# Performance work log

Hardware: AMD Instinct MI355X
Metric: run time of the kernel (lower is better)

Reference implementation:

```python
import jax, jax.numpy as jnp
import numpy as np

N = 16384      # total atoms (8 proteins x ~2048)
E = 524288     # N * max_neighbors(32)
B = 8          # graphs
F_IN = 26      # 20 residue types + 6 atom types
D = 128        # node_dim
H = 256        # hidden_dim
OUT = 64       # output_dim
L = 4          # n_layers
N_RBF = 16
CUTOFF = 10.0


def setup_inputs() -> dict:
    key = jax.random.key(0)
    ks = jax.random.split(key, 24)
    s = 0.05
    inp = {
        "positions": jax.random.normal(ks[0], (N, 3), jnp.float32) * 10.0,
        "node_features": jax.random.normal(ks[1], (N, F_IN), jnp.float32),
        "edge_index": jax.random.randint(ks[2], (2, E), 0, N, jnp.int32),
        "batch": jnp.sort(jax.random.randint(ks[3], (N,), 0, B, jnp.int32)),
        # node embedding MLP
        "emb_W1": jax.random.normal(ks[4], (F_IN, D), jnp.float32) * s,
        "emb_b1": jnp.zeros((D,), jnp.float32),
        "emb_W2": jax.random.normal(ks[5], (D, D), jnp.float32) * s,
        "emb_b2": jnp.zeros((D,), jnp.float32),
        # per-layer message MLP: [2D + n_rbf] -> H -> D
        "msg_W1": jax.random.normal(ks[6], (L, 2 * D + N_RBF, H), jnp.float32) * s,
        "msg_b1": jnp.zeros((L, H), jnp.float32),
        "msg_W2": jax.random.normal(ks[7], (L, H, D), jnp.float32) * s,
        "msg_b2": jnp.zeros((L, D), jnp.float32),
        # per-layer update MLP: [2D] -> H -> D (residual)
        "upd_W1": jax.random.normal(ks[8], (L, 2 * D, H), jnp.float32) * s,
        "upd_b1": jnp.zeros((L, H), jnp.float32),
        "upd_W2": jax.random.normal(ks[9], (L, H, D), jnp.float32) * s,
        "upd_b2": jnp.zeros((L, D), jnp.float32),
        # readout MLP: D -> H -> OUT
        "r_W1": jax.random.normal(ks[10], (D, H), jnp.float32) * s,
        "r_b1": jnp.zeros((H,), jnp.float32),
        "r_W2": jax.random.normal(ks[11], (H, OUT), jnp.float32) * s,
        "r_b2": jnp.zeros((OUT,), jnp.float32),
    }
    return inp


def _mlp2(x, W1, b1, W2, b2):
    return jax.nn.silu(x @ W1 + b1) @ W2 + b2


def _edge_rbf(positions, src, dst):
    rel = positions[dst] - positions[src]                      # (E,3)
    d = jnp.sqrt(jnp.sum(rel * rel, axis=-1) + 1e-12)          # (E,)
    centers = jnp.linspace(0.0, CUTOFF, N_RBF, dtype=positions.dtype)
    width = CUTOFF / N_RBF
    rbf = jnp.exp(-((d[:, None] - centers) ** 2) / (2.0 * width * width))  # (E,n_rbf)
    env = 0.5 * (jnp.cos(jnp.pi * d / CUTOFF) + 1.0) * (d < CUTOFF)        # cosine cutoff
    return rbf * env[:, None]


def reference(positions, node_features, edge_index, batch,
              emb_W1, emb_b1, emb_W2, emb_b2,
              msg_W1, msg_b1, msg_W2, msg_b2,
              upd_W1, upd_b1, upd_W2, upd_b2,
              r_W1, r_b1, r_W2, r_b2):
    src, dst = edge_index[0], edge_index[1]
    h = _mlp2(node_features, emb_W1, emb_b1, emb_W2, emb_b2)   # (N,D)
    ef = _edge_rbf(positions, src, dst)                        # (E,n_rbf)
    for i in range(L):
        m_in = jnp.concatenate([h[src], h[dst], ef], axis=-1)  # (E,2D+n_rbf)
        m = _mlp2(m_in, msg_W1[i], msg_b1[i], msg_W2[i], msg_b2[i])  # (E,D)
        agg = jax.ops.segment_sum(m, dst, num_segments=N)      # (N,D)
        u_in = jnp.concatenate([h, agg], axis=-1)              # (N,2D)
        h = h + _mlp2(u_in, upd_W1[i], upd_b1[i], upd_W2[i], upd_b2[i])
    # mean readout per graph
    counts = jax.ops.segment_sum(jnp.ones((N,), h.dtype), batch, num_segments=B)
    g = jax.ops.segment_sum(h, batch, num_segments=B) / jnp.maximum(counts, 1.0)[:, None]
    return _mlp2(g, r_W1, r_b1, r_W2, r_b2)                    # (B,OUT)
```

## Files before the change

kernel.cpp:

```cpp
#include <hip/hip_runtime.h>
#include <math.h>

#define NATOMS 16384
#define NEDGES 524288
#define NLAYERS 4
#define TE 64

typedef __bf16 bf16x8 __attribute__((ext_vector_type(8)));
typedef __bf16 bf16x4 __attribute__((ext_vector_type(4)));
typedef __bf16 bf16x2 __attribute__((ext_vector_type(2)));
typedef float f32x4 __attribute__((ext_vector_type(4)));

__device__ __forceinline__ float silu_f(float x) {
  return x * __builtin_amdgcn_rcpf(1.0f + __expf(-x));
}

__global__ __launch_bounds__(1024) void scan_kernel(
    const int* __restrict__ counts, int* __restrict__ cursor,
    float* __restrict__ degf)
{
  __shared__ int s_tot[1024];
  int tid = threadIdx.x;
  int v[16];
  {
    const int4* cp = (const int4*)(counts + tid * 16);
    int4 a = cp[0], b = cp[1], c = cp[2], d = cp[3];
    v[0]=a.x; v[1]=a.y; v[2]=a.z; v[3]=a.w;
    v[4]=b.x; v[5]=b.y; v[6]=b.z; v[7]=b.w;
    v[8]=c.x; v[9]=c.y; v[10]=c.z; v[11]=c.w;
    v[12]=d.x; v[13]=d.y; v[14]=d.z; v[15]=d.w;
  }
  int tot = 0;
  #pragma unroll
  for (int i = 0; i < 16; i++) tot += v[i];
  s_tot[tid] = tot;
  __syncthreads();
  for (int off = 1; off < 1024; off <<= 1) {
    int t = (tid >= off) ? s_tot[tid - off] : 0;
    __syncthreads();
    s_tot[tid] += t;
    __syncthreads();
  }
  int run = s_tot[tid] - tot;
  #pragma unroll
  for (int i = 0; i < 16; i++) {
    cursor[tid * 16 + i] = run;
    degf[tid * 16 + i] = (float)v[i];
    run += v[i];
  }
}

__global__ __launch_bounds__(256) void scatter_rbf_kernel(
    const int* __restrict__ src, const int* __restrict__ dst,
    int* __restrict__ cursor, const float* __restrict__ pos,
    int* __restrict__ esrc, int* __restrict__ edst,
    __bf16* __restrict__ efb)
{
  int e = blockIdx.x * 256 + threadIdx.x;
  int s = src[e], d = dst[e];
  int p = atomicAdd(&cursor[d], 1);
  esrc[p] = s;
  edst[p] = d;
  float dx = pos[d * 3 + 0] - pos[s * 3 + 0];
  float dy = pos[d * 3 + 1] - pos[s * 3 + 1];
  float dz = pos[d * 3 + 2] - pos[s * 3 + 2];
  float dist = sqrtf(dx * dx + dy * dy + dz * dz + 1e-12f);
  float env = (dist < 10.0f)
                  ? 0.5f * (cosf(3.14159265358979f * dist * 0.1f) + 1.0f)
                  : 0.0f;
  bf16x8 o0, o1;
  #pragma unroll
  for (int i = 0; i < 16; i++) {
    float c = (10.0f / 15.0f) * (float)i;
    float t = dist - c;
    float v = env * __expf(-t * t * 1.28f);
    if (i < 8) o0[i] = (__bf16)v; else o1[i - 8] = (__bf16)v;
  }
  *(bf16x8*)(efb + (size_t)p * 16 + 0) = o0;
  *(bf16x8*)(efb + (size_t)p * 16 + 8) = o1;
}

#define NB_PREP (801 * NLAYERS)
#define NB_HIST (NEDGES / 256)
#define NB_EMB  (NATOMS / 2)

__global__ __launch_bounds__(256) void front_kernel(
    const float* __restrict__ mW1, const float* __restrict__ mW2,
    const float* __restrict__ uW1, const float* __restrict__ uW2,
    const float* __restrict__ mb2,
    __bf16* __restrict__ W1at, __bf16* __restrict__ W1bt,
    __bf16* __restrict__ B2c, __bf16* __restrict__ uW1ft,
    __bf16* __restrict__ uW2t, float* __restrict__ b2u,
    const int* __restrict__ dstI, int* __restrict__ counts,
    const float* __restrict__ x, const float* __restrict__ eW1,
    const float* __restrict__ eb1, const float* __restrict__ eW2,
    const float* __restrict__ eb2, float* __restrict__ h,
    __bf16* __restrict__ hb)
{
  __shared__ float xs[2][26];
  __shared__ float hid[2][132];
  int bxf = blockIdx.x, tid = threadIdx.x;

  if (bxf < NB_PREP) {
    long l = bxf / 801;
    int bx = bxf - (int)l * 801;
    if (bx < 128) {
      int i = bx * 256 + tid;
      int n = i >> 7, k = i & 127;
      W1at[l * (256L * 128) + i] = (__bf16)mW1[l * (272L * 256) + (size_t)k * 256 + n];
    } else if (bx < 256) {
      int i = (bx - 128) * 256 + tid;
      int n = i >> 7, k = i & 127;
      W1bt[l * (256L * 128) + i] = (__bf16)mW1[l * (272L * 256) + (size_t)(128 + k) * 256 + n];
    } else if (bx < 288) {
      int i = (bx - 256) * 256 + tid;
      int c = i >> 5, k = i & 31;
      float v = (k < 16) ? mW1[l * (272L * 256) + (size_t)(256 + k) * 256 + c] : 0.0f;
      B2c[l * (256L * 32) + i] = (__bf16)v;
    } else if (bx < 672) {
      int k = bx - 288;
      int n = tid;
      float v;
      if (k < 128) {
        v = uW1[l * 65536 + (size_t)k * 256 + n];
      } else {
        int r = k - 128;
        v = 0.0f;
        for (int j = 0; j < 128; j++)
          v += mW2[(l * 256 + r) * 128 + j] * uW1[l * 65536 + (size_t)(128 + j) * 256 + n];
      }
      uW1ft[l * (256L * 384) + (size_t)n * 384 + k] = (__bf16)v;
    } else if (bx < 800) {
      int i = (bx - 672) * 256 + tid;
      int n = i >> 8, k = i & 255;
      uW2t[l * (128L * 256) + i] = (__bf16)uW2[l * (256L * 128) + (size_t)k * 128 + n];
    } else {
      int c = tid;
      float acc = 0.0f;
      for (int j = 0; j < 128; j++)
        acc += mb2[l * 128 + j] * uW1[l * 65536 + (size_t)(128 + j) * 256 + c];
      b2u[l * 256 + c] = acc;
    }
  } else if (bxf < NB_PREP + NB_HIST) {
    int e = (bxf - NB_PREP) * 256 + tid;
    atomicAdd(&counts[dstI[e]], 1);
  } else {
    int nb = bxf - (NB_PREP + NB_HIST);
    int hf = tid >> 7, j = tid & 127;
    int n = nb * 2 + hf;
    if (j < 26) xs[hf][j] = x[(size_t)n * 26 + j];
    __syncthreads();
    float acc = eb1[j];
    #pragma unroll
    for (int k = 0; k < 26; k++) acc += xs[hf][k] * eW1[k * 128 + j];
    hid[hf][j] = silu_f(acc);
    __syncthreads();
    float acc2 = eb2[j];
    #pragma unroll 8
    for (int k = 0; k < 128; k++) acc2 += hid[hf][k] * eW2[k * 128 + j];
    h[(size_t)n * 128 + j] = acc2;
    hb[(size_t)n * 128 + j] = (__bf16)acc2;
  }
}

__global__ __launch_bounds__(256) void zprep_kernel(
    const __bf16* __restrict__ hb, const float* __restrict__ b1,
    const __bf16* __restrict__ W1at, const __bf16* __restrict__ W1bt,
    __bf16* __restrict__ z1b, __bf16* __restrict__ z2b, float* __restrict__ aggH)
{
  __shared__ __bf16 s_n[64][136];
  int tid = threadIdx.x, n0 = blockIdx.x * 64;
  {
    int n = tid >> 2, t4 = tid & 3;
    const bf16x8* hr = (const bf16x8*)(hb + (size_t)(n0 + n) * 128);
    #pragma unroll
    for (int i = 0; i < 4; i++)
      *(bf16x8*)&s_n[n][t4 * 8 + 32 * i] = hr[t4 + 4 * i];
  }
  {
    float4 zz = make_float4(0.f, 0.f, 0.f, 0.f);
    float4* ap = (float4*)(aggH + (size_t)n0 * 256);
    for (int i = tid; i < 64 * 256 / 4; i += 256) ap[i] = zz;
  }
  __syncthreads();
  const int wv = tid >> 6, ln = tid & 63, lc = ln & 15, qd = ln >> 4;
  for (int cp = 0; cp < 2; cp++) {
    f32x4 aA[4][2], aB[4][2];
    #pragma unroll
    for (int nt = 0; nt < 2; nt++) {
      float bv = b1[cp * 128 + wv * 32 + nt * 16 + lc];
      #pragma unroll
      for (int mt = 0; mt < 4; mt++) {
        aA[mt][nt][0] = 0.f; aA[mt][nt][1] = 0.f;
        aA[mt][nt][2] = 0.f; aA[mt][nt][3] = 0.f;
        aB[mt][nt][0] = bv; aB[mt][nt][1] = bv;
        aB[mt][nt][2] = bv; aB[mt][nt][3] = bv;
      }
    }
    #pragma unroll
    for (int kt = 0; kt < 4; kt++) {
      bf16x8 af[4];
      #pragma unroll
      for (int mt = 0; mt < 4; mt++)
        af[mt] = *(const bf16x8*)&s_n[mt * 16 + lc][kt * 32 + qd * 8];
      bf16x8 bwA[2], bwB[2];
      #pragma unroll
      for (int nt = 0; nt < 2; nt++) {
        int c = cp * 128 + wv * 32 + nt * 16 + lc;
        bwA[nt] = *(const bf16x8*)(W1at + (size_t)c * 128 + kt * 32 + qd * 8);
        bwB[nt] = *(const bf16x8*)(W1bt + (size_t)c * 128 + kt * 32 + qd * 8);
      }
      #pragma unroll
      for (int mt = 0; mt < 4; mt++)
        #pragma unroll
        for (int nt = 0; nt < 2; nt++) {
          aA[mt][nt] = __builtin_amdgcn_mfma_f32_16x16x32_bf16(af[mt], bwA[nt], aA[mt][nt], 0, 0, 0);
          aB[mt][nt] = __builtin_amdgcn_mfma_f32_16x16x32_bf16(af[mt], bwB[nt], aB[mt][nt], 0, 0, 0);
        }
    }
    #pragma unroll
    for (int mt = 0; mt < 4; mt++)
      #pragma unroll
      for (int nt = 0; nt < 2; nt++) {
        int c = cp * 128 + wv * 32 + nt * 16 + lc;
        #pragma unroll
        for (int r = 0; r < 4; r++) {
          int n = n0 + mt * 16 + qd * 4 + r;
          z1b[(size_t)n * 256 + c] = (__bf16)aA[mt][nt][r];
          z2b[(size_t)n * 256 + c] = (__bf16)aB[mt][nt][r];
        }
      }
  }
}

#define MS_EF_OFF   33792
#define MS_SRC_OFF  36864
#define MS_DST_OFF  37120
#define MS_MASK_OFF 37376
#define MS_BYTES    37392

__global__ __launch_bounds__(256, 4) void msg_mfma_kernel(
    const __bf16* __restrict__ z1b, const __bf16* __restrict__ z2b,
    const __bf16* __restrict__ efb,
    const int* __restrict__ esrc, const int* __restrict__ edst,
    const __bf16* __restrict__ B2c, float* __restrict__ aggH)
{
  __shared__ __align__(16) char smem[MS_BYTES];
  __bf16 (*s_hT)[66] = (__bf16(*)[66])(smem);
  __bf16 (*s_ef)[24] = (__bf16(*)[24])(smem + MS_EF_OFF);
  int* s_src = (int*)(smem + MS_SRC_OFF);
  int* s_dst = (int*)(smem + MS_DST_OFF);
  unsigned int* s_mask = (unsigned int*)(smem + MS_MASK_OFF);

  int tid = threadIdx.x, e0 = blockIdx.x * TE;

  if (tid < TE) {
    int d = edst[e0 + tid];
    s_dst[tid] = d;
    int dp = (tid == 0) ? (d ^ 1) : edst[e0 + tid - 1];
    unsigned long long mb = __ballot(d != dp);
    if (tid == 0) { s_mask[0] = (unsigned int)mb; s_mask[1] = (unsigned int)(mb >> 32); }
  } else if (tid < 2 * TE) {
    s_src[tid - TE] = esrc[e0 + tid - TE];
  }
  {
    int e = tid >> 2, t4 = tid & 3;
    if (t4 < 2)
      *(bf16x8*)&s_ef[e][t4 * 8] =
          *(const bf16x8*)(efb + (size_t)(e0 + e) * 16 + t4 * 8);
  }
  __syncthreads();

  const int wv = tid >> 6, ln = tid & 63, lc = ln & 15, qd = ln >> 4;

  bf16x8 bI;
  #pragma unroll
  for (int j = 0; j < 8; j++)
    bI[j] = (__bf16)((lc == (qd & 1) * 8 + j) ? 1.0f : 0.0f);

  const __bf16* pz[4];
  #pragma unroll
  for (int mt = 0; mt < 4; mt++) {
    int m = mt * 16 + lc;
    int row = (qd < 2) ? s_src[m] : s_dst[m];
    pz[mt] = ((qd < 2) ? z1b : z2b) + (size_t)row * 256 + (qd & 1) * 8;
  }

  #pragma unroll
  for (int hf = 0; hf < 2; hf++) {
    const int cb = hf * 128 + wv * 32;
    bf16x8 bw[2];
    #pragma unroll
    for (int nt = 0; nt < 2; nt++)
      bw[nt] = *(const bf16x8*)(B2c + (size_t)(cb + nt * 16 + lc) * 32 + qd * 8);

    #pragma unroll
    for (int mt = 0; mt < 4; mt++) {
      bf16x8 aef = *(const bf16x8*)&s_ef[mt * 16 + lc][(qd & 1) * 8];
      #pragma unroll
      for (int nt = 0; nt < 2; nt++) {
        bf16x8 az = *(const bf16x8*)(pz[mt] + cb + nt * 16);
        f32x4 z; z[0] = 0.f; z[1] = 0.f; z[2] = 0.f; z[3] = 0.f;
        f32x4 acc = __builtin_amdgcn_mfma_f32_16x16x32_bf16(az, bI, z, 0, 0, 0);
        acc = __builtin_amdgcn_mfma_f32_16x16x32_bf16(aef, bw[nt], acc, 0, 0, 0);
        bf16x2 p0, p1;
        p0[0] = (__bf16)silu_f(acc[0]); p0[1] = (__bf16)silu_f(acc[1]);
        p1[0] = (__bf16)silu_f(acc[2]); p1[1] = (__bf16)silu_f(acc[3]);
        __bf16* wp = &s_hT[cb + nt * 16 + lc][mt * 16 + qd * 4];
        *(bf16x2*)wp = p0;
        *(bf16x2*)(wp + 2) = p1;
      }
    }
  }
  __syncthreads();

  {
    const unsigned int mlo = __builtin_amdgcn_readfirstlane(s_mask[0]);
    const unsigned int mhi = __builtin_amdgcn_readfirstlane(s_mask[1]);
    int j = tid;
    float acc = 0.0f;
    int cur = s_dst[0];
    #pragma unroll 8
    for (int i = 0; i < 64; i += 2) {
      bf16x2 p = *(const bf16x2*)&s_hT[j][i];
      bool b0 = (i < 32) ? ((mlo >> i) & 1u) : ((mhi >> (i - 32)) & 1u);
      int i1 = i + 1;
      bool b1 = (i1 < 32) ? ((mlo >> i1) & 1u) : ((mhi >> (i1 - 32)) & 1u);
      if (i > 0 && b0) {
        atomicAdd(&aggH[(size_t)cur * 256 + j], acc);
        acc = 0.0f; cur = s_dst[i];
      }
      acc += (float)p[0];
      if (b1) {
        atomicAdd(&aggH[(size_t)cur * 256 + j], acc);
        acc = 0.0f; cur = s_dst[i1];
      }
      acc += (float)p[1];
    }
    atomicAdd(&aggH[(size_t)cur * 256 + j], acc);
  }
}

__global__ __launch_bounds__(512, 2) void upd_mfma_kernel(
    float* __restrict__ h, __bf16* __restrict__ hb,
    float* __restrict__ aggH, const float* __restrict__ degf,
    const __bf16* __restrict__ uW1ft, const float* __restrict__ b1,
    const float* __restrict__ b2u,
    const __bf16* __restrict__ uW2t, const float* __restrict__ b2,
    int do_z, const float* __restrict__ nb1,
    const __bf16* __restrict__ nW1at, const __bf16* __restrict__ nW1bt,
    __bf16* __restrict__ z1b, __bf16* __restrict__ z2b)
{
  __shared__ __bf16 s_u[64][392];
  __shared__ __bf16 s_uh[64][264];
  int tid = threadIdx.x, n0 = blockIdx.x * 64;
  {
    int n = tid >> 3, t8 = tid & 7;
    const bf16x8* hr = (const bf16x8*)(hb + (size_t)(n0 + n) * 128);
    #pragma unroll
    for (int i = 0; i < 2; i++)
      *(bf16x8*)&s_u[n][t8 * 8 + 64 * i] = hr[t8 + 8 * i];
    const float* sr = aggH + (size_t)(n0 + n) * 256;
    #pragma unroll
    for (int i = 0; i < 4; i++) {
      int col = t8 * 8 + i * 64;
      float4 a = *(const float4*)(sr + col);
      float4 b = *(const float4*)(sr + col + 4);
      bf16x8 o;
      o[0] = (__bf16)a.x; o[1] = (__bf16)a.y; o[2] = (__bf16)a.z; o[3] = (__bf16)a.w;
      o[4] = (__bf16)b.x; o[5] = (__bf16)b.y; o[6] = (__bf16)b.z; o[7] = (__bf16)b.w;
      *(bf16x8*)&s_u[n][128 + col] = o;
    }
  }
  __syncthreads();
  const int wv = tid >> 6, ln = tid & 63, lc = ln & 15, qd = ln >> 4;

  float dg[4][4];
  #pragma unroll
  for (int mt = 0; mt < 4; mt++)
    #pragma unroll
    for (int r = 0; r < 4; r++)
      dg[mt][r] = degf[n0 + mt * 16 + qd * 4 + r];

  {
    f32x4 acc1[4][2];
    #pragma unroll
    for (int nt = 0; nt < 2; nt++) {
      int c = wv * 32 + nt * 16 + lc;
      float bv = b1[c];
      float b2uv = b2u[c];
      #pragma unroll
      for (int mt = 0; mt < 4; mt++)
        #pragma unroll
        for (int r = 0; r < 4; r++)
          acc1[mt][nt][r] = bv + dg[mt][r] * b2uv;
    }
    #pragma unroll
    for (int kt = 0; kt < 12; kt++) {
      bf16x8 af[4];
      #pragma unroll
      for (int mt = 0; mt < 4; mt++)
        af[mt] = *(const bf16x8*)&s_u[mt * 16 + lc][kt * 32 + qd * 8];
      bf16x8 bw[2];
      #pragma unroll
      for (int nt = 0; nt < 2; nt++)
        bw[nt] = *(const bf16x8*)(uW1ft +
                 (size_t)(wv * 32 + nt * 16 + lc) * 384 + kt * 32 + qd * 8);
      #pragma unroll
      for (int mt = 0; mt < 4; mt++)
        #pragma unroll
        for (int nt = 0; nt < 2; nt++)
          acc1[mt][nt] = __builtin_amdgcn_mfma_f32_16x16x32_bf16(af[mt], bw[nt], acc1[mt][nt], 0, 0, 0);
    }
    #pragma unroll
    for (int mt = 0; mt < 4; mt++)
      #pragma unroll
      for (int nt = 0; nt < 2; nt++) {
        int cc = wv * 32 + nt * 16 + lc;
        #pragma unroll
        for (int r = 0; r < 4; r++)
          s_uh[mt * 16 + qd * 4 + r][cc] = (__bf16)silu_f(acc1[mt][nt][r]);
      }
  }
  __syncthreads();

  const int ow = wv * 16 + lc;
  f32x4 acc2[4];
  {
    float bv = b2[ow];
    #pragma unroll
    for (int mt = 0; mt < 4; mt++) {
      acc2[mt][0] = bv; acc2[mt][1] = bv; acc2[mt][2] = bv; acc2[mt][3] = bv;
    }
  }
  #pragma unroll
  for (int kt = 0; kt < 8; kt++) {
    bf16x8 a2[4];
    #pragma unroll
    for (int mt = 0; mt < 4; mt++)
      a2[mt] = *(const bf16x8*)&s_uh[mt * 16 + lc][kt * 32 + qd * 8];
    bf16x8 b2w = *(const bf16x8*)(uW2t + (size_t)ow * 256 + kt * 32 + qd * 8);
    #pragma unroll
    for (int mt = 0; mt < 4; mt++)
      acc2[mt] = __builtin_amdgcn_mfma_f32_16x16x32_bf16(a2[mt], b2w, acc2[mt], 0, 0, 0);
  }

  #pragma unroll
  for (int mt = 0; mt < 4; mt++)
    #pragma unroll
    for (int r = 0; r < 4; r++) {
      int n = n0 + mt * 16 + qd * 4 + r;
      float v = h[(size_t)n * 128 + ow] + acc2[mt][r];
      h[(size_t)n * 128 + ow] = v;
      hb[(size_t)n * 128 + ow] = (__bf16)v;
    }

  if (do_z) {
    __syncthreads();
    {
      float4 zz = make_float4(0.f, 0.f, 0.f, 0.f);
      float4* ap = (float4*)(aggH + (size_t)n0 * 256);
      for (int i = tid; i < 64 * 256 / 4; i += 512) ap[i] = zz;
      int n = tid >> 3, t8 = tid & 7;
      const bf16x8* hr = (const bf16x8*)(hb + (size_t)(n0 + n) * 128);
      #pragma unroll
      for (int i = 0; i < 2; i++)
        *(bf16x8*)&s_u[n][t8 * 8 + 64 * i] = hr[t8 + 8 * i];
    }
    __syncthreads();
    f32x4 aA[4][2], aB[4][2];
    #pragma unroll
    for (int nt = 0; nt < 2; nt++) {
      float bv = nb1[wv * 32 + nt * 16 + lc];
      #pragma unroll
      for (int mt = 0; mt < 4; mt++) {
        aA[mt][nt][0] = 0.f; aA[mt][nt][1] = 0.f;
        aA[mt][nt][2] = 0.f; aA[mt][nt][3] = 0.f;
        aB[mt][nt][0] = bv; aB[mt][nt][1] = bv;
        aB[mt][nt][2] = bv; aB[mt][nt][3] = bv;
      }
    }
    #pragma unroll
    for (int kt = 0; kt < 4; kt++) {
      bf16x8 af[4];
      #pragma unroll
      for (int mt = 0; mt < 4; mt++)
        af[mt] = *(const bf16x8*)&s_u[mt * 16 + lc][kt * 32 + qd * 8];
      bf16x8 bwA[2], bwB[2];
      #pragma unroll
      for (int nt = 0; nt < 2; nt++) {
        int c = wv * 32 + nt * 16 + lc;
        bwA[nt] = *(const bf16x8*)(nW1at + (size_t)c * 128 + kt * 32 + qd * 8);
        bwB[nt] = *(const bf16x8*)(nW1bt + (size_t)c * 128 + kt * 32 + qd * 8);
      }
      #pragma unroll
      for (int mt = 0; mt < 4; mt++)
        #pragma unroll
        for (int nt = 0; nt < 2; nt++) {
          aA[mt][nt] = __builtin_amdgcn_mfma_f32_16x16x32_bf16(af[mt], bwA[nt], aA[mt][nt], 0, 0, 0);
          aB[mt][nt] = __builtin_amdgcn_mfma_f32_16x16x32_bf16(af[mt], bwB[nt], aB[mt][nt], 0, 0, 0);
        }
    }
    #pragma unroll
    for (int mt = 0; mt < 4; mt++)
      #pragma unroll
      for (int nt = 0; nt < 2; nt++) {
        int c = wv * 32 + nt * 16 + lc;
        #pragma unroll
        for (int r = 0; r < 4; r++) {
          int n = n0 + mt * 16 + qd * 4 + r;
          z1b[(size_t)n * 256 + c] = (__bf16)aA[mt][nt][r];
          z2b[(size_t)n * 256 + c] = (__bf16)aB[mt][nt][r];
        }
      }
  }
}

__global__ __launch_bounds__(128) void readout_sum_kernel(
    const float* __restrict__ h, const int* __restrict__ batch,
    float* __restrict__ gsum, float* __restrict__ gcnt)
{
  int j = threadIdx.x;
  int n0 = blockIdx.x * 128;
  float acc = 0.f, cacc = 0.f;
  int cur = batch[n0];
  for (int i = 0; i < 128; i++) {
    int b = batch[n0 + i];
    if (b != cur) {
      atomicAdd(&gsum[cur * 128 + j], acc);
      if (j == 0) atomicAdd(&gcnt[cur], cacc);
      acc = 0.f; cacc = 0.f; cur = b;
    }
    acc += h[(size_t)(n0 + i) * 128 + j];
    cacc += 1.f;
  }
  atomicAdd(&gsum[cur * 128 + j], acc);
  if (j == 0) atomicAdd(&gcnt[cur], cacc);
}

__global__ __launch_bounds__(256) void readout_mlp_kernel(
    const float* __restrict__ gsum, const float* __restrict__ gcnt,
    const float* __restrict__ W1, const float* __restrict__ b1,
    const float* __restrict__ W2, const float* __restrict__ b2,
    float* __restrict__ out)
{
  __shared__ float g[8][128];
  __shared__ float hid[8][256];
  int tid = threadIdx.x;
  for (int i = tid; i < 8 * 128; i += 256) {
    int b = i >> 7, c = i & 127;
    g[b][c] = gsum[i] / fmaxf(gcnt[b], 1.0f);
  }
  __syncthreads();
  {
    float bb = b1[tid];
    float a[8];
    #pragma unroll
    for (int b = 0; b < 8; b++) a[b] = bb;
    for (int k = 0; k < 128; k++) {
      float w = W1[k * 256 + tid];
      #pragma unroll
      for (int b = 0; b < 8; b++) a[b] += g[b][k] * w;
    }
    #pragma unroll
    for (int b = 0; b < 8; b++) hid[b][tid] = silu_f(a[b]);
  }
  __syncthreads();
  int j = tid & 63, bg = tid >> 6;
  float a0 = b2[j], a1 = b2[j];
  for (int k = 0; k < 256; k++) {
    float w = W2[k * 64 + j];
    a0 += hid[bg * 2 + 0][k] * w;
    a1 += hid[bg * 2 + 1][k] * w;
  }
  out[(bg * 2 + 0) * 64 + j] = a0;
  out[(bg * 2 + 1) * 64 + j] = a1;
}

extern "C" void kernel_launch(void* const* d_in, const int* in_sizes, int n_in,
                              void* d_out, int out_size, void* d_ws, size_t ws_size,
                              hipStream_t stream) {
  const float* pos   = (const float*)d_in[0];
  const float* xfeat = (const float*)d_in[1];
  const int*   eidx  = (const int*)d_in[2];
  const int*   batch = (const int*)d_in[3];
  const float* eW1 = (const float*)d_in[4];
  const float* eb1 = (const float*)d_in[5];
  const float* eW2 = (const float*)d_in[6];
  const float* eb2 = (const float*)d_in[7];
  const float* mW1 = (const float*)d_in[8];
  const float* mb1 = (const float*)d_in[9];
  const float* mW2 = (const float*)d_in[10];
  const float* mb2 = (const float*)d_in[11];
  const float* uW1 = (const float*)d_in[12];
  const float* ub1 = (const float*)d_in[13];
  const float* uW2 = (const float*)d_in[14];
  const float* ub2 = (const float*)d_in[15];
  const float* rW1 = (const float*)d_in[16];
  const float* rb1 = (const float*)d_in[17];
  const float* rW2 = (const float*)d_in[18];
  const float* rb2 = (const float*)d_in[19];

  const int* srcI = eidx;
  const int* dstI = eidx + NEDGES;

  char* base = (char*)d_ws;
  float* h    = (float*)base;  base += (size_t)NATOMS * 128 * 4;
  float* aggH = (float*)base;  base += (size_t)NATOMS * 256 * 4;
  __bf16* z1b = (__bf16*)base; base += (size_t)NATOMS * 256 * 2;
  __bf16* z2b = (__bf16*)base; base += (size_t)NATOMS * 256 * 2;
  __bf16* hb  = (__bf16*)base; base += (size_t)NATOMS * 128 * 2;
  __bf16* efb = (__bf16*)base; base += (size_t)NEDGES * 16 * 2;
  __bf16* W1at = (__bf16*)base; base += (size_t)NLAYERS * 256 * 128 * 2;
  __bf16* W1bt = (__bf16*)base; base += (size_t)NLAYERS * 256 * 128 * 2;
  __bf16* B2c  = (__bf16*)base; base += (size_t)NLAYERS * 256 * 32 * 2;
  __bf16* uW1ft = (__bf16*)base; base += (size_t)NLAYERS * 256 * 384 * 2;
  __bf16* uW2t = (__bf16*)base; base += (size_t)NLAYERS * 128 * 256 * 2;
  float* b2u  = (float*)base;  base += (size_t)NLAYERS * 256 * 4;
  float* degf = (float*)base;  base += (size_t)NATOMS * 4;
  float* gsum = (float*)base;  base += 8 * 128 * 4;
  float* gcnt = (float*)base;  base += 8 * 4;
  int* counts = (int*)base;    base += (size_t)NATOMS * 4;
  int* cursor = (int*)base;    base += (size_t)NATOMS * 4;
  int* esrc   = (int*)base;    base += (size_t)NEDGES * 4;
  int* edst   = (int*)base;    base += (size_t)NEDGES * 4;

  hipMemsetAsync(counts, 0, NATOMS * sizeof(int), stream);

  front_kernel<<<NB_PREP + NB_HIST + NB_EMB, 256, 0, stream>>>(
      mW1, mW2, uW1, uW2, mb2, W1at, W1bt, B2c, uW1ft, uW2t, b2u,
      dstI, counts, xfeat, eW1, eb1, eW2, eb2, h, hb);

  scan_kernel<<<1, 1024, 0, stream>>>(counts, cursor, degf);
  scatter_rbf_kernel<<<NEDGES / 256, 256, 0, stream>>>(
      srcI, dstI, cursor, pos, esrc, edst, efb);

  zprep_kernel<<<NATOMS / 64, 256, 0, stream>>>(
      hb, mb1, W1at, W1bt, z1b, z2b, aggH);

  for (int l = 0; l < NLAYERS; l++) {
    int ln = (l < NLAYERS - 1) ? (l + 1) : l;
    msg_mfma_kernel<<<NEDGES / TE, 256, 0, stream>>>(
        z1b, z2b, efb, esrc, edst,
        B2c + (size_t)l * 256 * 32, aggH);
    upd_mfma_kernel<<<NATOMS / 64, 512, 0, stream>>>(
        h, hb, aggH, degf,
        uW1ft + (size_t)l * 256 * 384, ub1 + (size_t)l * 256,
        b2u + (size_t)l * 256,
        uW2t + (size_t)l * 128 * 256, ub2 + (size_t)l * 128,
        (l < NLAYERS - 1) ? 1 : 0,
        mb1 + (size_t)ln * 256,
        W1at + (size_t)ln * 256 * 128, W1bt + (size_t)ln * 256 * 128,
        z1b, z2b);
  }

  hipMemsetAsync(gsum, 0, (8 * 128 + 8) * sizeof(float), stream);
  readout_sum_kernel<<<NATOMS / 128, 128, 0, stream>>>(h, batch, gsum, gcnt);
  readout_mlp_kernel<<<1, 256, 0, stream>>>(gsum, gcnt, rW1, rb1, rW2, rb2,
                                            (float*)d_out);
}
```

Measured before the change: 637.0 us.

## Reduce message segments via MFMA indicator matmul instead of LDS transpose scan

Replaces the LDS-staged transpose and per-column serial segment scan in the message kernel with an in-register reduction. ds_bpermute reshapes the activated message tiles into MFMA operands, and a one-hot segment-indicator matrix is multiplied against them to sum edges that share a destination. The results are then atomically added per segment. This removes the large LDS buffer and a block barrier, which allows occupancy to rise to 5 blocks per CU. In exchange it adds bpermute traffic and extra MFMAs, and the loop trip count now depends on how many distinct destinations each tile holds.

```diff
diff --git a/kernel.cpp b/kernel.cpp
--- a/kernel.cpp
+++ b/kernel.cpp
@@ -233,24 +233,18 @@
   }
 }
 
-#define MS_EF_OFF   33792
-#define MS_SRC_OFF  36864
-#define MS_DST_OFF  37120
-#define MS_MASK_OFF 37376
-#define MS_BYTES    37392
-
-__global__ __launch_bounds__(256, 4) void msg_mfma_kernel(
+__global__ __launch_bounds__(256, 5) void msg_mfma_kernel(
     const __bf16* __restrict__ z1b, const __bf16* __restrict__ z2b,
     const __bf16* __restrict__ efb,
     const int* __restrict__ esrc, const int* __restrict__ edst,
     const __bf16* __restrict__ B2c, float* __restrict__ aggH)
 {
-  __shared__ __align__(16) char smem[MS_BYTES];
-  __bf16 (*s_hT)[66] = (__bf16(*)[66])(smem);
-  __bf16 (*s_ef)[24] = (__bf16(*)[24])(smem + MS_EF_OFF);
-  int* s_src = (int*)(smem + MS_SRC_OFF);
-  int* s_dst = (int*)(smem + MS_DST_OFF);
-  unsigned int* s_mask = (unsigned int*)(smem + MS_MASK_OFF);
+  __shared__ __align__(16) __bf16 s_ef[TE][24];
+  __shared__ int s_src[TE];
+  __shared__ int s_dst[TE];
+  __shared__ int s_dseg[TE];
+  __shared__ unsigned char s_seg[TE];
+  __shared__ int s_nseg;
 
   int tid = threadIdx.x, e0 = blockIdx.x * TE;
 
@@ -259,7 +253,11 @@
     s_dst[tid] = d;
     int dp = (tid == 0) ? (d ^ 1) : edst[e0 + tid - 1];
     unsigned long long mb = __ballot(d != dp);
-    if (tid == 0) { s_mask[0] = (unsigned int)mb; s_mask[1] = (unsigned int)(mb >> 32); }
+    unsigned long long below = mb & (~0ull >> (63 - tid));
+    int seg = (int)__popcll(below) - 1;
+    s_seg[tid] = (unsigned char)seg;
+    if (d != dp) s_dseg[seg] = d;
+    if (tid == 0) s_nseg = (int)__popcll(mb);
   } else if (tid < 2 * TE) {
     s_src[tid - TE] = esrc[e0 + tid - TE];
   }
@@ -273,6 +271,9 @@
 
   const int wv = tid >> 6, ln = tid & 63, lc = ln & 15, qd = ln >> 4;
 
+  const int nseg = __builtin_amdgcn_readfirstlane(s_nseg);
+  const int nst = (nseg + 15) >> 4;
+
   bf16x8 bI;
   #pragma unroll
   for (int j = 0; j < 8; j++)
@@ -286,58 +287,91 @@
     pz[mt] = ((qd < 2) ? z1b : z2b) + (size_t)row * 256 + (qd & 1) * 8;
   }
 
+  bf16x8 aef[4];
+  #pragma unroll
+  for (int mt = 0; mt < 4; mt++)
+    aef[mt] = *(const bf16x8*)&s_ef[mt * 16 + lc][(qd & 1) * 8];
+
+  unsigned int segk[2][2];
+  #pragma unroll
+  for (int kf = 0; kf < 2; kf++) {
+    const unsigned int* sp = (const unsigned int*)&s_seg[kf * 32 + qd * 8];
+    segk[kf][0] = sp[0];
+    segk[kf][1] = sp[1];
+  }
+  bf16x8 ind0[2];
+  #pragma unroll
+  for (int kf = 0; kf < 2; kf++)
+    #pragma unroll
+    for (int j = 0; j < 8; j++) {
+      int b = (segk[kf][j >> 2] >> (8 * (j & 3))) & 255;
+      ind0[kf][j] = (b == lc) ? (__bf16)1.0f : (__bf16)0.0f;
+    }
+
+  int rb0[4];
+  #pragma unroll
+  for (int r = 0; r < 4; r++)
+    rb0[r] = s_dseg[qd * 4 + r];
+
+  const int aw0 = 4 * lc + (qd & 1) * 128;
+  const int aw1 = aw0 + 64;
+
   #pragma unroll
   for (int hf = 0; hf < 2; hf++) {
-    const int cb = hf * 128 + wv * 32;
-    bf16x8 bw[2];
-    #pragma unroll
-    for (int nt = 0; nt < 2; nt++)
-      bw[nt] = *(const bf16x8*)(B2c + (size_t)(cb + nt * 16 + lc) * 32 + qd * 8);
-
-    #pragma unroll
-    for (int mt = 0; mt < 4; mt++) {
-      bf16x8 aef = *(const bf16x8*)&s_ef[mt * 16 + lc][(qd & 1) * 8];
-      #pragma unroll
-      for (int nt = 0; nt < 2; nt++) {
-        bf16x8 az = *(const bf16x8*)(pz[mt] + cb + nt * 16);
+    #pragma unroll
+    for (int nt = 0; nt < 2; nt++) {
+      const int cb = hf * 128 + wv * 32 + nt * 16;
+      bf16x8 bw = *(const bf16x8*)(B2c + (size_t)(cb + lc) * 32 + qd * 8);
+      int pr[4][2];
+      #pragma unroll
+      for (int mt = 0; mt < 4; mt++) {
+        bf16x8 az = *(const bf16x8*)(pz[mt] + cb);
         f32x4 z; z[0] = 0.f; z[1] = 0.f; z[2] = 0.f; z[3] = 0.f;
         f32x4 acc = __builtin_amdgcn_mfma_f32_16x16x32_bf16(az, bI, z, 0, 0, 0);
-        acc = __builtin_amdgcn_mfma_f32_16x16x32_bf16(aef, bw[nt], acc, 0, 0, 0);
+        acc = __builtin_amdgcn_mfma_f32_16x16x32_bf16(aef[mt], bw, acc, 0, 0, 0);
         bf16x2 p0, p1;
         p0[0] = (__bf16)silu_f(acc[0]); p0[1] = (__bf16)silu_f(acc[1]);
         p1[0] = (__bf16)silu_f(acc[2]); p1[1] = (__bf16)silu_f(acc[3]);
-        __bf16* wp = &s_hT[cb + nt * 16 + lc][mt * 16 + qd * 4];
-        *(bf16x2*)wp = p0;
-        *(bf16x2*)(wp + 2) = p1;
-      }
-    }
-  }
-  __syncthreads();
-
-  {
-    const unsigned int mlo = __builtin_amdgcn_readfirstlane(s_mask[0]);
-    const unsigned int mhi = __builtin_amdgcn_readfirstlane(s_mask[1]);
-    int j = tid;
-    float acc = 0.0f;
-    int cur = s_dst[0];
-    #pragma unroll 8
-    for (int i = 0; i < 64; i += 2) {
-      bf16x2 p = *(const bf16x2*)&s_hT[j][i];
-      bool b0 = (i < 32) ? ((mlo >> i) & 1u) : ((mhi >> (i - 32)) & 1u);
-      int i1 = i + 1;
-      bool b1 = (i1 < 32) ? ((mlo >> i1) & 1u) : ((mhi >> (i1 - 32)) & 1u);
-      if (i > 0 && b0) {
-        atomicAdd(&aggH[(size_t)cur * 256 + j], acc);
-        acc = 0.0f; cur = s_dst[i];
-      }
-      acc += (float)p[0];
-      if (b1) {
-        atomicAdd(&aggH[(size_t)cur * 256 + j], acc);
-        acc = 0.0f; cur = s_dst[i1];
-      }
-      acc += (float)p[1];
-    }
-    atomicAdd(&aggH[(size_t)cur * 256 + j], acc);
+        pr[mt][0] = __builtin_bit_cast(int, p0);
+        pr[mt][1] = __builtin_bit_cast(int, p1);
+      }
+      union { bf16x8 v; int d[4]; } fr[2];
+      #pragma unroll
+      for (int kf = 0; kf < 2; kf++)
+        #pragma unroll
+        for (int w = 0; w < 4; w++) {
+          int addr = (w < 2) ? aw0 : aw1;
+          int lo = __builtin_amdgcn_ds_bpermute(addr, pr[kf * 2 + 0][w & 1]);
+          int hi = __builtin_amdgcn_ds_bpermute(addr, pr[kf * 2 + 1][w & 1]);
+          fr[kf].d[w] = (qd < 2) ? lo : hi;
+        }
+      for (int st = 0; st < nst; st++) {
+        bf16x8 i0, i1;
+        if (st == 0) {
+          i0 = ind0[0]; i1 = ind0[1];
+        } else {
+          int tgt = st * 16 + lc;
+          #pragma unroll
+          for (int j = 0; j < 8; j++) {
+            int b0 = (segk[0][j >> 2] >> (8 * (j & 3))) & 255;
+            int b1 = (segk[1][j >> 2] >> (8 * (j & 3))) & 255;
+            i0[j] = (b0 == tgt) ? (__bf16)1.0f : (__bf16)0.0f;
+            i1[j] = (b1 == tgt) ? (__bf16)1.0f : (__bf16)0.0f;
+          }
+        }
+        f32x4 s; s[0] = 0.f; s[1] = 0.f; s[2] = 0.f; s[3] = 0.f;
+        s = __builtin_amdgcn_mfma_f32_16x16x32_bf16(i0, fr[0].v, s, 0, 0, 0);
+        s = __builtin_amdgcn_mfma_f32_16x16x32_bf16(i1, fr[1].v, s, 0, 0, 0);
+        #pragma unroll
+        for (int r = 0; r < 4; r++) {
+          int seg = st * 16 + qd * 4 + r;
+          if (seg < nseg) {
+            int row = (st == 0) ? rb0[r] : s_dseg[seg];
+            atomicAdd(&aggH[(size_t)row * 256 + cb + lc], s[r]);
+          }
+        }
+      }
+    }
   }
 }
 
```

After: 709.1 us. 11.3% more time.

## Halve message-kernel shared staging and split segment reduction across halves

Applied to the files above, without the earlier changes.

The message kernel now stages only 128 hidden columns at a time in shared memory (about 18KB instead of 37KB) and processes the two column halves sequentially, with an extra barrier between them. The segmented scatter-add is restructured so each thread handles 128 columns times 32 edges per half, which yields more atomic flushes at the 32-edge boundary. The edge-feature A fragments are hoisted out of the loop. Occupancy is raised to 7 blocks per SM via launch bounds, trading extra synchronization and somewhat more atomics for better latency hiding.

```diff
diff --git a/kernel.cpp b/kernel.cpp
--- a/kernel.cpp
+++ b/kernel.cpp
@@ -233,24 +233,17 @@
   }
 }
 
-#define MS_EF_OFF   33792
-#define MS_SRC_OFF  36864
-#define MS_DST_OFF  37120
-#define MS_MASK_OFF 37376
-#define MS_BYTES    37392
-
-__global__ __launch_bounds__(256, 4) void msg_mfma_kernel(
+__global__ __launch_bounds__(256, 7) void msg_mfma_kernel(
     const __bf16* __restrict__ z1b, const __bf16* __restrict__ z2b,
     const __bf16* __restrict__ efb,
     const int* __restrict__ esrc, const int* __restrict__ edst,
     const __bf16* __restrict__ B2c, float* __restrict__ aggH)
 {
-  __shared__ __align__(16) char smem[MS_BYTES];
-  __bf16 (*s_hT)[66] = (__bf16(*)[66])(smem);
-  __bf16 (*s_ef)[24] = (__bf16(*)[24])(smem + MS_EF_OFF);
-  int* s_src = (int*)(smem + MS_SRC_OFF);
-  int* s_dst = (int*)(smem + MS_DST_OFF);
-  unsigned int* s_mask = (unsigned int*)(smem + MS_MASK_OFF);
+  __shared__ __align__(16) __bf16 s_hT[128][70];
+  __shared__ __align__(16) __bf16 s_ef[TE][24];
+  __shared__ int s_src[TE];
+  __shared__ int s_dst[TE];
+  __shared__ unsigned int s_mask[2];
 
   int tid = threadIdx.x, e0 = blockIdx.x * TE;
 
@@ -286,58 +279,59 @@
     pz[mt] = ((qd < 2) ? z1b : z2b) + (size_t)row * 256 + (qd & 1) * 8;
   }
 
+  bf16x8 aef[4];
+  #pragma unroll
+  for (int mt = 0; mt < 4; mt++)
+    aef[mt] = *(const bf16x8*)&s_ef[mt * 16 + lc][(qd & 1) * 8];
+
+  const int sj = tid & 127;
+  const int srow0 = (tid >> 7) * 32;
+  const unsigned int smask = __builtin_amdgcn_readfirstlane(s_mask[tid >> 7]);
+
   #pragma unroll
   for (int hf = 0; hf < 2; hf++) {
-    const int cb = hf * 128 + wv * 32;
-    bf16x8 bw[2];
-    #pragma unroll
-    for (int nt = 0; nt < 2; nt++)
-      bw[nt] = *(const bf16x8*)(B2c + (size_t)(cb + nt * 16 + lc) * 32 + qd * 8);
-
-    #pragma unroll
-    for (int mt = 0; mt < 4; mt++) {
-      bf16x8 aef = *(const bf16x8*)&s_ef[mt * 16 + lc][(qd & 1) * 8];
-      #pragma unroll
-      for (int nt = 0; nt < 2; nt++) {
-        bf16x8 az = *(const bf16x8*)(pz[mt] + cb + nt * 16);
+    if (hf) __syncthreads();
+
+    #pragma unroll
+    for (int nt = 0; nt < 2; nt++) {
+      const int cb = hf * 128 + wv * 32 + nt * 16;
+      bf16x8 bw = *(const bf16x8*)(B2c + (size_t)(cb + lc) * 32 + qd * 8);
+      #pragma unroll
+      for (int mt = 0; mt < 4; mt++) {
+        bf16x8 az = *(const bf16x8*)(pz[mt] + cb);
         f32x4 z; z[0] = 0.f; z[1] = 0.f; z[2] = 0.f; z[3] = 0.f;
         f32x4 acc = __builtin_amdgcn_mfma_f32_16x16x32_bf16(az, bI, z, 0, 0, 0);
-        acc = __builtin_amdgcn_mfma_f32_16x16x32_bf16(aef, bw[nt], acc, 0, 0, 0);
+        acc = __builtin_amdgcn_mfma_f32_16x16x32_bf16(aef[mt], bw, acc, 0, 0, 0);
         bf16x2 p0, p1;
         p0[0] = (__bf16)silu_f(acc[0]); p0[1] = (__bf16)silu_f(acc[1]);
         p1[0] = (__bf16)silu_f(acc[2]); p1[1] = (__bf16)silu_f(acc[3]);
-        __bf16* wp = &s_hT[cb + nt * 16 + lc][mt * 16 + qd * 4];
+        __bf16* wp = &s_hT[wv * 32 + nt * 16 + lc][mt * 16 + qd * 4];
         *(bf16x2*)wp = p0;
         *(bf16x2*)(wp + 2) = p1;
       }
     }
-  }
-  __syncthreads();
-
-  {
-    const unsigned int mlo = __builtin_amdgcn_readfirstlane(s_mask[0]);
-    const unsigned int mhi = __builtin_amdgcn_readfirstlane(s_mask[1]);
-    int j = tid;
-    float acc = 0.0f;
-    int cur = s_dst[0];
-    #pragma unroll 8
-    for (int i = 0; i < 64; i += 2) {
-      bf16x2 p = *(const bf16x2*)&s_hT[j][i];
-      bool b0 = (i < 32) ? ((mlo >> i) & 1u) : ((mhi >> (i - 32)) & 1u);
-      int i1 = i + 1;
-      bool b1 = (i1 < 32) ? ((mlo >> i1) & 1u) : ((mhi >> (i1 - 32)) & 1u);
-      if (i > 0 && b0) {
-        atomicAdd(&aggH[(size_t)cur * 256 + j], acc);
-        acc = 0.0f; cur = s_dst[i];
-      }
-      acc += (float)p[0];
-      if (b1) {
-        atomicAdd(&aggH[(size_t)cur * 256 + j], acc);
-        acc = 0.0f; cur = s_dst[i1];
-      }
-      acc += (float)p[1];
-    }
-    atomicAdd(&aggH[(size_t)cur * 256 + j], acc);
+    __syncthreads();
+
+    {
+      const int gcol = hf * 128 + sj;
+      float acc = 0.0f;
+      int cur = s_dst[srow0];
+      #pragma unroll 8
+      for (int i = 0; i < 32; i += 2) {
+        bf16x2 p = *(const bf16x2*)&s_hT[sj][srow0 + i];
+        if (i > 0 && ((smask >> i) & 1u)) {
+          atomicAdd(&aggH[(size_t)cur * 256 + gcol], acc);
+          acc = 0.0f; cur = s_dst[srow0 + i];
+        }
+        acc += (float)p[0];
+        if ((smask >> (i + 1)) & 1u) {
+          atomicAdd(&aggH[(size_t)cur * 256 + gcol], acc);
+          acc = 0.0f; cur = s_dst[srow0 + i + 1];
+        }
+        acc += (float)p[1];
+      }
+      atomicAdd(&aggH[(size_t)cur * 256 + gcol], acc);
+    }
   }
 }
 
```

After: 599.2 us. 1.06x faster.
